# Kernel tuning notes

Hardware: AMD Instinct MI355X
Metric: run time of the kernel (lower is better)

The kernel has to match this reference:

```python
import jax, jax.numpy as jnp
import numpy as np

T, B, I, H = 2048, 256, 64, 128


def setup_inputs() -> dict:
    key = jax.random.key(0)
    ks = jax.random.split(key, 12)
    s_i = 1.0 / np.sqrt(I)
    s_h = 1.0 / np.sqrt(H)
    return {
        "x": jax.random.normal(ks[0], (T, B, I), dtype=jnp.float32),
        # input->hidden kernels (with bias), flax GRUCell naming ir/iz/in
        "Wir": jax.random.normal(ks[1], (I, H), dtype=jnp.float32) * s_i,
        "Wiz": jax.random.normal(ks[2], (I, H), dtype=jnp.float32) * s_i,
        "Win": jax.random.normal(ks[3], (I, H), dtype=jnp.float32) * s_i,
        "bir": jnp.zeros((H,), dtype=jnp.float32),
        "biz": jnp.zeros((H,), dtype=jnp.float32),
        "bin": jnp.zeros((H,), dtype=jnp.float32),
        # hidden->hidden kernels: hr/hz no bias, hn has bias (flax GRUCell)
        "Whr": jax.random.normal(ks[4], (H, H), dtype=jnp.float32) * s_h,
        "Whz": jax.random.normal(ks[5], (H, H), dtype=jnp.float32) * s_h,
        "Whn": jax.random.normal(ks[6], (H, H), dtype=jnp.float32) * s_h,
        "bhn": jnp.zeros((H,), dtype=jnp.float32),
        # classifier Linear(H, 1)
        "Wc": jax.random.normal(ks[7], (H, 1), dtype=jnp.float32) * s_h,
        "bc": jnp.zeros((1,), dtype=jnp.float32),
    }


def reference(x, Wir, Wiz, Win, bir, biz, bin, Whr, Whz, Whn, bhn, Wc, bc):
    # GRU scan over time (time-major), flax GRUCell math:
    # r = sig(x Wir + bir + h Whr); z = sig(x Wiz + biz + h Whz)
    def step(h, xt):
        r = jax.nn.sigmoid(xt @ Wir + bir + h @ Whr)
        z = jax.nn.sigmoid(xt @ Wiz + biz + h @ Whz)
        n = jnp.tanh(xt @ Win + bin + r * (h @ Whn + bhn))
        h_new = (1.0 - z) * n + z * h
        return h_new, h_new

    h0 = jnp.zeros((x.shape[1], Whr.shape[0]), dtype=x.dtype)
    _, hs = jax.lax.scan(step, h0, x)  # hs: [T, B, H]
    return jax.nn.sigmoid(hs @ Wc + bc)  # [T, B, 1]
```

## Files before the change

kernel.cpp:

```cpp
#include <hip/hip_runtime.h>

#define TT 2048
#define BB 256
#define II 64
#define HH 128
#define CHP 16
#define NCH (TT / CHP)
#define GXS 532

typedef __fp16 f16;
typedef __fp16 h2  __attribute__((ext_vector_type(2)));
typedef __fp16 v8h __attribute__((ext_vector_type(8)));
typedef float  v4f __attribute__((ext_vector_type(4)));

union HI { int i; h2 h; };
__device__ __forceinline__ h2  i2h(int v) { HI u; u.i = v; return u.h; }
__device__ __forceinline__ int h2i(h2 v)  { HI u; u.h = v; return u.i; }

__device__ __forceinline__ float fsig(float x) {
  return __builtin_amdgcn_rcpf(1.0f + __expf(-x));
}
__device__ __forceinline__ float ftanh(float x) {
  return 1.0f - 2.0f * __builtin_amdgcn_rcpf(1.0f + __expf(2.0f * x));
}

__device__ __forceinline__ void bar_lgkm() {
  asm volatile("s_waitcnt lgkmcnt(0)\n\ts_barrier" ::: "memory");
}

template <int CLS>
__global__ __launch_bounds__(512, 1) void gru_mfma(
    const float* __restrict__ x,
    const float* __restrict__ Wir, const float* __restrict__ Wiz, const float* __restrict__ Win,
    const float* __restrict__ bir, const float* __restrict__ biz, const float* __restrict__ bin_,
    const float* __restrict__ Whr, const float* __restrict__ Whz, const float* __restrict__ Whn,
    const float* __restrict__ bhn, const float* __restrict__ Wc,  const float* __restrict__ bc,
    float* __restrict__ hh, float* __restrict__ out)
{
  const int t = threadIdx.x, b = blockIdx.x;
  const int w = t >> 6;
  const int l = t & 63;
  const int q = l >> 4;
  const int r = l & 15;
  const int nc = 16 * w + r;

  __shared__ __attribute__((aligned(16))) f16   hbuf[2][HH];
  __shared__ __attribute__((aligned(16))) f16   xch[2][CHP][72];
  __shared__ __attribute__((aligned(16))) float gxb[2][CHP][GXS];
  __shared__ float cpart[2][128];

  v8h br_[6], bz_[6], bnh_[4], bnx_[2];
  for (int kt = 0; kt < 6; ++kt) {
    v8h vr, vz;
    for (int j = 0; j < 8; ++j) {
      const int kg = 32 * kt + 8 * q + j;
      vr[j] = (f16)((kg < HH) ? Whr[kg * HH + nc] : Wir[(kg - HH) * HH + nc]);
      vz[j] = (f16)((kg < HH) ? Whz[kg * HH + nc] : Wiz[(kg - HH) * HH + nc]);
    }
    br_[kt] = vr; bz_[kt] = vz;
  }
  for (int kt = 0; kt < 4; ++kt) {
    v8h v;
    for (int j = 0; j < 8; ++j) v[j] = (f16)Whn[(32 * kt + 8 * q + j) * HH + nc];
    bnh_[kt] = v;
  }
  for (int kt = 0; kt < 2; ++kt) {
    v8h v;
    for (int j = 0; j < 8; ++j) v[j] = (f16)Win[(32 * kt + 8 * q + j) * HH + nc];
    bnx_[kt] = v;
  }

  const float birc = bir[nc], bizc = biz[nc], binc = bin_[nc], bhnc = bhn[nc];
  float wc = 0.f, bc0 = 0.f;
  if (CLS == 1) { wc = Wc[nc]; bc0 = bc[0]; }

  auto precomp = [&](int pn, v8h ax0, v8h ax1) {
    v4f cr = {birc, birc, birc, birc};
    v4f cz = {bizc, bizc, bizc, bizc};
    v4f cn = {binc, binc, binc, binc};
    cr = __builtin_amdgcn_mfma_f32_16x16x32_f16(ax0, br_[4],  cr, 0, 0, 0);
    cz = __builtin_amdgcn_mfma_f32_16x16x32_f16(ax0, bz_[4],  cz, 0, 0, 0);
    cn = __builtin_amdgcn_mfma_f32_16x16x32_f16(ax0, bnx_[0], cn, 0, 0, 0);
    cr = __builtin_amdgcn_mfma_f32_16x16x32_f16(ax1, br_[5],  cr, 0, 0, 0);
    cz = __builtin_amdgcn_mfma_f32_16x16x32_f16(ax1, bz_[5],  cz, 0, 0, 0);
    cn = __builtin_amdgcn_mfma_f32_16x16x32_f16(ax1, bnx_[1], cn, 0, 0, 0);
    #pragma unroll
    for (int j = 0; j < 4; ++j) {
      v4f pk; pk[0] = cr[j]; pk[1] = cz[j]; pk[2] = cn[j]; pk[3] = 0.f;
      *(v4f*)&gxb[pn][4 * q + j][nc * 4] = pk;
    }
  };

  const int xrow = t >> 5, xcol = (t & 31) * 2;
  float2 xr;
  {
    float2 xA = *(const float2*)(x + ((size_t)(0   + xrow) * BB + b) * II + xcol);
    float2 xB = *(const float2*)(x + ((size_t)(CHP + xrow) * BB + b) * II + xcol);
    if (t < HH) { hbuf[0][t] = (f16)0.f; hbuf[1][t] = (f16)0.f; }
    *(int*)&xch[0][xrow][xcol] = h2i(__builtin_amdgcn_cvt_pkrtz(xA.x, xA.y));
    __syncthreads();
    {
      v8h a0x = *(const v8h*)&xch[0][r][8 * q];
      v8h a1x = *(const v8h*)&xch[0][r][32 + 8 * q];
      precomp(0, a0x, a1x);
    }
    *(int*)&xch[1][xrow][xcol] = h2i(__builtin_amdgcn_cvt_pkrtz(xB.x, xB.y));
    __syncthreads();
  }

  v4f gp = *(const v4f*)&gxb[0][0][nc * 4];

  v8h af[4] = {};
  float hst = 0.f;
  float* hps = (CLS == 0) ? (hh + (size_t)b * HH + nc) : nullptr;

  for (int c = 0; c < NCH; ++c) {
    const int p = c & 1;
    const bool pc = (c + 1 < NCH);
    const bool ld = (c + 2 < NCH);

    v8h ax0 = {}, ax1 = {};
    if (pc) {
      ax0 = *(const v8h*)&xch[p ^ 1][r][8 * q];
      ax1 = *(const v8h*)&xch[p ^ 1][r][32 + 8 * q];
    }
    if (ld) {
      xr = *(const float2*)(x + ((size_t)((c + 2) * CHP + xrow) * BB + b) * II + xcol);
    }

    #pragma unroll
    for (int sc = 0; sc < CHP; ++sc) {
      const int s = c * CHP + sc;
      const int cur = sc & 1, nxt = cur ^ 1;

      if (r == 0) {
        af[0] = *(const v8h*)&hbuf[cur][8 * q];
        af[1] = *(const v8h*)&hbuf[cur][32 + 8 * q];
        af[2] = *(const v8h*)&hbuf[cur][64 + 8 * q];
        af[3] = *(const v8h*)&hbuf[cur][96 + 8 * q];
      }

      float cred = 0.f;
      if (CLS == 1 && w == 7 && (sc > 0 || c > 0))
        cred = cpart[nxt][l] + cpart[nxt][64 + l];

      const v4f vz0 = {0.f, 0.f, 0.f, 0.f};
      v4f ar0, ar1, an0, an1, az0, az1;
      ar0 = __builtin_amdgcn_mfma_f32_16x16x32_f16(af[0], br_[0], vz0, 0, 0, 0);
      ar1 = __builtin_amdgcn_mfma_f32_16x16x32_f16(af[2], br_[2], vz0, 0, 0, 0);
      ar0 = __builtin_amdgcn_mfma_f32_16x16x32_f16(af[1], br_[1], ar0, 0, 0, 0);
      ar1 = __builtin_amdgcn_mfma_f32_16x16x32_f16(af[3], br_[3], ar1, 0, 0, 0);
      an0 = __builtin_amdgcn_mfma_f32_16x16x32_f16(af[0], bnh_[0], vz0, 0, 0, 0);
      an1 = __builtin_amdgcn_mfma_f32_16x16x32_f16(af[2], bnh_[2], vz0, 0, 0, 0);
      an0 = __builtin_amdgcn_mfma_f32_16x16x32_f16(af[1], bnh_[1], an0, 0, 0, 0);
      an1 = __builtin_amdgcn_mfma_f32_16x16x32_f16(af[3], bnh_[3], an1, 0, 0, 0);
      az0 = __builtin_amdgcn_mfma_f32_16x16x32_f16(af[0], bz_[0], vz0, 0, 0, 0);
      az1 = __builtin_amdgcn_mfma_f32_16x16x32_f16(af[2], bz_[2], vz0, 0, 0, 0);
      az0 = __builtin_amdgcn_mfma_f32_16x16x32_f16(af[1], bz_[1], az0, 0, 0, 0);
      az1 = __builtin_amdgcn_mfma_f32_16x16x32_f16(af[3], bz_[3], az1, 0, 0, 0);

      const v4f g = gp;
      if (sc < CHP - 1) {
        gp = *(const v4f*)&gxb[p][sc + 1][nc * 4];
      } else if (c + 1 < NCH) {
        gp = *(const v4f*)&gxb[p ^ 1][0][nc * 4];
      }

      if (q == 0) {
        const float arS = ar0[0] + ar1[0] + g[0];
        const float anS = an0[0] + an1[0] + bhnc;
        const float rr  = fsig(arS);
        const float nn  = ftanh(g[2] + rr * anS);
        const float azS = az0[0] + az1[0] + g[1];
        const float zz  = fsig(azS);
        hst = nn + zz * (hst - nn);
        hbuf[nxt][nc] = (f16)hst;
        if (CLS == 0) *hps = hst;
        if (CLS == 1) cpart[cur][nc] = hst * wc;
      }
      if (CLS == 0) hps += BB * HH;

      if (CLS == 1 && w == 7 && (sc > 0 || c > 0)) {
        cred += __shfl_xor(cred, 1, 64);
        cred += __shfl_xor(cred, 2, 64);
        cred += __shfl_xor(cred, 4, 64);
        cred += __shfl_xor(cred, 8, 64);
        cred += __shfl_xor(cred, 16, 64);
        cred += __shfl_xor(cred, 32, 64);
        if (l == 0) out[(size_t)(s - 1) * BB + b] = fsig(cred + bc0);
      }

      if (sc == 0 && pc) precomp(p ^ 1, ax0, ax1);

      if (sc == CHP - 1 && ld) {
        *(int*)&xch[p][xrow][xcol] = h2i(__builtin_amdgcn_cvt_pkrtz(xr.x, xr.y));
      }

      bar_lgkm();
    }
  }

  if (CLS == 1 && w == 7) {
    float cred = cpart[1][l] + cpart[1][64 + l];
    cred += __shfl_xor(cred, 1, 64);
    cred += __shfl_xor(cred, 2, 64);
    cred += __shfl_xor(cred, 4, 64);
    cred += __shfl_xor(cred, 8, 64);
    cred += __shfl_xor(cred, 16, 64);
    cred += __shfl_xor(cred, 32, 64);
    if (l == 0) out[(size_t)(TT - 1) * BB + b] = fsig(cred + bc0);
  }
}

__global__ __launch_bounds__(256) void gru_cls(
    const float* __restrict__ hh, const float* __restrict__ Wc,
    const float* __restrict__ bc, float* __restrict__ out)
{
  const int t  = threadIdx.x;
  const int g4 = t & 3;
  const size_t row = (size_t)blockIdx.x * 64 + (t >> 2);
  const float* hp = hh + row * HH + 32 * g4;
  const float* wp = Wc + 32 * g4;
  float acc = 0.f;
  #pragma unroll
  for (int i = 0; i < 8; ++i) {
    v4f h4 = *(const v4f*)(hp + 4 * i);
    v4f w4 = *(const v4f*)(wp + 4 * i);
    acc += h4[0] * w4[0] + h4[1] * w4[1] + h4[2] * w4[2] + h4[3] * w4[3];
  }
  acc += __shfl_xor(acc, 1, 64);
  acc += __shfl_xor(acc, 2, 64);
  if (g4 == 0) out[row] = fsig(acc + bc[0]);
}

extern "C" void kernel_launch(void* const* d_in, const int* in_sizes, int n_in,
                              void* d_out, int out_size, void* d_ws, size_t ws_size,
                              hipStream_t stream) {
  const float* x    = (const float*)d_in[0];
  const float* Wir  = (const float*)d_in[1];
  const float* Wiz  = (const float*)d_in[2];
  const float* Win  = (const float*)d_in[3];
  const float* bir  = (const float*)d_in[4];
  const float* biz  = (const float*)d_in[5];
  const float* bin_ = (const float*)d_in[6];
  const float* Whr  = (const float*)d_in[7];
  const float* Whz  = (const float*)d_in[8];
  const float* Whn  = (const float*)d_in[9];
  const float* bhn  = (const float*)d_in[10];
  const float* Wc   = (const float*)d_in[11];
  const float* bc   = (const float*)d_in[12];
  float* out = (float*)d_out;

  const size_t need = (size_t)TT * BB * HH * sizeof(float);
  if (d_ws != nullptr && ws_size >= need) {
    float* hh = (float*)d_ws;
    gru_mfma<0><<<dim3(BB), dim3(512), 0, stream>>>(
        x, Wir, Wiz, Win, bir, biz, bin_, Whr, Whz, Whn, bhn, Wc, bc, hh, out);
    gru_cls<<<dim3((TT * BB) / 64), dim3(256), 0, stream>>>(hh, Wc, bc, out);
  } else {
    gru_mfma<1><<<dim3(BB), dim3(512), 0, stream>>>(
        x, Wir, Wiz, Win, bir, biz, bin_, Whr, Whz, Whn, bhn, Wc, bc, nullptr, out);
  }
}
```

Measured before the change: 951.6 us.

## Spread input precompute across steps, fold log2e into weights, store hidden in fp16

The per-chunk input projection (six MFMAs plus four LDS stores) used to run in one step. It is now spread over the first ten steps of each chunk so the serial recurrence sees a smaller burst at each barrier. The weights and biases are pre-scaled by log2(e) or 2·log2(e) so the gates can call v_exp_f32 directly without a multiply. The hidden-state workspace is written as fp16, which halves the global traffic in both the recurrence and the classifier kernels at some cost in precision. The recurrent MFMAs are also reordered to interleave the r and n chains.

New measurement: 866.6 us. -8.9%, faster.

```diff
diff --git a/kernel.cpp b/kernel.cpp
--- a/kernel.cpp
+++ b/kernel.cpp
@@ -8,6 +8,9 @@
 #define NCH (TT / CHP)
 #define GXS 532
 
+#define LOG2E  1.4426950408889634f
+#define LOG2E2 2.8853900817779268f
+
 typedef __fp16 f16;
 typedef __fp16 h2  __attribute__((ext_vector_type(2)));
 typedef __fp16 v8h __attribute__((ext_vector_type(8)));
@@ -17,11 +20,11 @@
 __device__ __forceinline__ h2  i2h(int v) { HI u; u.i = v; return u.h; }
 __device__ __forceinline__ int h2i(h2 v)  { HI u; u.h = v; return u.i; }
 
+__device__ __forceinline__ float fexp2(float x) {
+  float r; asm("v_exp_f32 %0, %1" : "=v"(r) : "v"(x)); return r;
+}
 __device__ __forceinline__ float fsig(float x) {
   return __builtin_amdgcn_rcpf(1.0f + __expf(-x));
-}
-__device__ __forceinline__ float ftanh(float x) {
-  return 1.0f - 2.0f * __builtin_amdgcn_rcpf(1.0f + __expf(2.0f * x));
 }
 
 __device__ __forceinline__ void bar_lgkm() {
@@ -35,7 +38,7 @@
     const float* __restrict__ bir, const float* __restrict__ biz, const float* __restrict__ bin_,
     const float* __restrict__ Whr, const float* __restrict__ Whz, const float* __restrict__ Whn,
     const float* __restrict__ bhn, const float* __restrict__ Wc,  const float* __restrict__ bc,
-    float* __restrict__ hh, float* __restrict__ out)
+    f16* __restrict__ hh, float* __restrict__ out)
 {
   const int t = threadIdx.x, b = blockIdx.x;
   const int w = t >> 6;
@@ -54,27 +57,28 @@
     v8h vr, vz;
     for (int j = 0; j < 8; ++j) {
       const int kg = 32 * kt + 8 * q + j;
-      vr[j] = (f16)((kg < HH) ? Whr[kg * HH + nc] : Wir[(kg - HH) * HH + nc]);
-      vz[j] = (f16)((kg < HH) ? Whz[kg * HH + nc] : Wiz[(kg - HH) * HH + nc]);
+      vr[j] = (f16)(LOG2E * ((kg < HH) ? Whr[kg * HH + nc] : Wir[(kg - HH) * HH + nc]));
+      vz[j] = (f16)(LOG2E * ((kg < HH) ? Whz[kg * HH + nc] : Wiz[(kg - HH) * HH + nc]));
     }
     br_[kt] = vr; bz_[kt] = vz;
   }
   for (int kt = 0; kt < 4; ++kt) {
     v8h v;
-    for (int j = 0; j < 8; ++j) v[j] = (f16)Whn[(32 * kt + 8 * q + j) * HH + nc];
+    for (int j = 0; j < 8; ++j) v[j] = (f16)(LOG2E2 * Whn[(32 * kt + 8 * q + j) * HH + nc]);
     bnh_[kt] = v;
   }
   for (int kt = 0; kt < 2; ++kt) {
     v8h v;
-    for (int j = 0; j < 8; ++j) v[j] = (f16)Win[(32 * kt + 8 * q + j) * HH + nc];
+    for (int j = 0; j < 8; ++j) v[j] = (f16)(LOG2E2 * Win[(32 * kt + 8 * q + j) * HH + nc]);
     bnx_[kt] = v;
   }
 
-  const float birc = bir[nc], bizc = biz[nc], binc = bin_[nc], bhnc = bhn[nc];
+  const float birc = LOG2E * bir[nc],  bizc = LOG2E * biz[nc];
+  const float binc = LOG2E2 * bin_[nc], bhnc = LOG2E2 * bhn[nc];
   float wc = 0.f, bc0 = 0.f;
   if (CLS == 1) { wc = Wc[nc]; bc0 = bc[0]; }
 
-  auto precomp = [&](int pn, v8h ax0, v8h ax1) {
+  auto precomp_full = [&](int pn, v8h ax0, v8h ax1) {
     v4f cr = {birc, birc, birc, birc};
     v4f cz = {bizc, bizc, bizc, bizc};
     v4f cn = {binc, binc, binc, binc};
@@ -102,7 +106,7 @@
     {
       v8h a0x = *(const v8h*)&xch[0][r][8 * q];
       v8h a1x = *(const v8h*)&xch[0][r][32 + 8 * q];
-      precomp(0, a0x, a1x);
+      precomp_full(0, a0x, a1x);
     }
     *(int*)&xch[1][xrow][xcol] = h2i(__builtin_amdgcn_cvt_pkrtz(xB.x, xB.y));
     __syncthreads();
@@ -112,7 +116,8 @@
 
   v8h af[4] = {};
   float hst = 0.f;
-  float* hps = (CLS == 0) ? (hh + (size_t)b * HH + nc) : nullptr;
+  f16* hup = (CLS == 0) ? (hh + (size_t)b * HH) : nullptr;
+  v4f cpr, cpz, cpn;
 
   for (int c = 0; c < NCH; ++c) {
     const int p = c & 1;
@@ -140,24 +145,47 @@
         af[3] = *(const v8h*)&hbuf[cur][96 + 8 * q];
       }
 
+      if (pc) {
+        if (sc == 0) {
+          v4f ir = {birc, birc, birc, birc};
+          cpr = __builtin_amdgcn_mfma_f32_16x16x32_f16(ax0, br_[4], ir, 0, 0, 0);
+        } else if (sc == 1) {
+          v4f iz = {bizc, bizc, bizc, bizc};
+          cpz = __builtin_amdgcn_mfma_f32_16x16x32_f16(ax0, bz_[4], iz, 0, 0, 0);
+        } else if (sc == 2) {
+          v4f in_ = {binc, binc, binc, binc};
+          cpn = __builtin_amdgcn_mfma_f32_16x16x32_f16(ax0, bnx_[0], in_, 0, 0, 0);
+        } else if (sc == 3) {
+          cpr = __builtin_amdgcn_mfma_f32_16x16x32_f16(ax1, br_[5], cpr, 0, 0, 0);
+        } else if (sc == 4) {
+          cpz = __builtin_amdgcn_mfma_f32_16x16x32_f16(ax1, bz_[5], cpz, 0, 0, 0);
+        } else if (sc == 5) {
+          cpn = __builtin_amdgcn_mfma_f32_16x16x32_f16(ax1, bnx_[1], cpn, 0, 0, 0);
+        } else if (sc >= 6 && sc < 10) {
+          const int j = sc - 6;
+          v4f pk; pk[0] = cpr[j]; pk[1] = cpz[j]; pk[2] = cpn[j]; pk[3] = 0.f;
+          *(v4f*)&gxb[p ^ 1][4 * q + j][nc * 4] = pk;
+        }
+      }
+
       float cred = 0.f;
       if (CLS == 1 && w == 7 && (sc > 0 || c > 0))
         cred = cpart[nxt][l] + cpart[nxt][64 + l];
 
       const v4f vz0 = {0.f, 0.f, 0.f, 0.f};
       v4f ar0, ar1, an0, an1, az0, az1;
-      ar0 = __builtin_amdgcn_mfma_f32_16x16x32_f16(af[0], br_[0], vz0, 0, 0, 0);
-      ar1 = __builtin_amdgcn_mfma_f32_16x16x32_f16(af[2], br_[2], vz0, 0, 0, 0);
-      ar0 = __builtin_amdgcn_mfma_f32_16x16x32_f16(af[1], br_[1], ar0, 0, 0, 0);
-      ar1 = __builtin_amdgcn_mfma_f32_16x16x32_f16(af[3], br_[3], ar1, 0, 0, 0);
+      ar0 = __builtin_amdgcn_mfma_f32_16x16x32_f16(af[0], br_[0],  vz0, 0, 0, 0);
       an0 = __builtin_amdgcn_mfma_f32_16x16x32_f16(af[0], bnh_[0], vz0, 0, 0, 0);
+      ar0 = __builtin_amdgcn_mfma_f32_16x16x32_f16(af[1], br_[1],  ar0, 0, 0, 0);
+      an0 = __builtin_amdgcn_mfma_f32_16x16x32_f16(af[1], bnh_[1], an0, 0, 0, 0);
+      ar1 = __builtin_amdgcn_mfma_f32_16x16x32_f16(af[2], br_[2],  vz0, 0, 0, 0);
       an1 = __builtin_amdgcn_mfma_f32_16x16x32_f16(af[2], bnh_[2], vz0, 0, 0, 0);
-      an0 = __builtin_amdgcn_mfma_f32_16x16x32_f16(af[1], bnh_[1], an0, 0, 0, 0);
+      ar1 = __builtin_amdgcn_mfma_f32_16x16x32_f16(af[3], br_[3],  ar1, 0, 0, 0);
       an1 = __builtin_amdgcn_mfma_f32_16x16x32_f16(af[3], bnh_[3], an1, 0, 0, 0);
-      az0 = __builtin_amdgcn_mfma_f32_16x16x32_f16(af[0], bz_[0], vz0, 0, 0, 0);
-      az1 = __builtin_amdgcn_mfma_f32_16x16x32_f16(af[2], bz_[2], vz0, 0, 0, 0);
-      az0 = __builtin_amdgcn_mfma_f32_16x16x32_f16(af[1], bz_[1], az0, 0, 0, 0);
-      az1 = __builtin_amdgcn_mfma_f32_16x16x32_f16(af[3], bz_[3], az1, 0, 0, 0);
+      az0 = __builtin_amdgcn_mfma_f32_16x16x32_f16(af[0], bz_[0],  vz0, 0, 0, 0);
+      az1 = __builtin_amdgcn_mfma_f32_16x16x32_f16(af[2], bz_[2],  vz0, 0, 0, 0);
+      az0 = __builtin_amdgcn_mfma_f32_16x16x32_f16(af[1], bz_[1],  az0, 0, 0, 0);
+      az1 = __builtin_amdgcn_mfma_f32_16x16x32_f16(af[3], bz_[3],  az1, 0, 0, 0);
 
       const v4f g = gp;
       if (sc < CHP - 1) {
@@ -168,17 +196,18 @@
 
       if (q == 0) {
         const float arS = ar0[0] + ar1[0] + g[0];
+        const float rr  = __builtin_amdgcn_rcpf(1.f + fexp2(-arS));
         const float anS = an0[0] + an1[0] + bhnc;
-        const float rr  = fsig(arS);
-        const float nn  = ftanh(g[2] + rr * anS);
+        const float nn  = 1.f - 2.f * __builtin_amdgcn_rcpf(1.f + fexp2(g[2] + rr * anS));
         const float azS = az0[0] + az1[0] + g[1];
-        const float zz  = fsig(azS);
+        const float zz  = __builtin_amdgcn_rcpf(1.f + fexp2(-azS));
         hst = nn + zz * (hst - nn);
-        hbuf[nxt][nc] = (f16)hst;
-        if (CLS == 0) *hps = hst;
+        const f16 hf = (f16)hst;
+        hbuf[nxt][nc] = hf;
+        if (CLS == 0) hup[nc] = hf;
         if (CLS == 1) cpart[cur][nc] = hst * wc;
       }
-      if (CLS == 0) hps += BB * HH;
+      if (CLS == 0) hup += BB * HH;
 
       if (CLS == 1 && w == 7 && (sc > 0 || c > 0)) {
         cred += __shfl_xor(cred, 1, 64);
@@ -189,8 +218,6 @@
         cred += __shfl_xor(cred, 32, 64);
         if (l == 0) out[(size_t)(s - 1) * BB + b] = fsig(cred + bc0);
       }
-
-      if (sc == 0 && pc) precomp(p ^ 1, ax0, ax1);
 
       if (sc == CHP - 1 && ld) {
         *(int*)&xch[p][xrow][xcol] = h2i(__builtin_amdgcn_cvt_pkrtz(xr.x, xr.y));
@@ -213,20 +240,21 @@
 }
 
 __global__ __launch_bounds__(256) void gru_cls(
-    const float* __restrict__ hh, const float* __restrict__ Wc,
+    const f16* __restrict__ hh, const float* __restrict__ Wc,
     const float* __restrict__ bc, float* __restrict__ out)
 {
   const int t  = threadIdx.x;
   const int g4 = t & 3;
   const size_t row = (size_t)blockIdx.x * 64 + (t >> 2);
-  const float* hp = hh + row * HH + 32 * g4;
+  const f16* hp = hh + row * HH + 32 * g4;
   const float* wp = Wc + 32 * g4;
   float acc = 0.f;
   #pragma unroll
-  for (int i = 0; i < 8; ++i) {
-    v4f h4 = *(const v4f*)(hp + 4 * i);
-    v4f w4 = *(const v4f*)(wp + 4 * i);
-    acc += h4[0] * w4[0] + h4[1] * w4[1] + h4[2] * w4[2] + h4[3] * w4[3];
+  for (int i = 0; i < 4; ++i) {
+    v8h h8 = *(const v8h*)(hp + 8 * i);
+    const float* wq = wp + 8 * i;
+    #pragma unroll
+    for (int j = 0; j < 8; ++j) acc += (float)h8[j] * wq[j];
   }
   acc += __shfl_xor(acc, 1, 64);
   acc += __shfl_xor(acc, 2, 64);
@@ -251,9 +279,9 @@
   const float* bc   = (const float*)d_in[12];
   float* out = (float*)d_out;
 
-  const size_t need = (size_t)TT * BB * HH * sizeof(float);
+  const size_t need = (size_t)TT * BB * HH * sizeof(f16);
   if (d_ws != nullptr && ws_size >= need) {
-    float* hh = (float*)d_ws;
+    f16* hh = (f16*)d_ws;
     gru_mfma<0><<<dim3(BB), dim3(512), 0, stream>>>(
         x, Wir, Wiz, Win, bir, biz, bin_, Whr, Whz, Whn, bhn, Wc, bc, hh, out);
     gru_cls<<<dim3((TT * BB) / 64), dim3(256), 0, stream>>>(hh, Wc, bc, out);
```
